# Kernel optimization log

Measured on AMD Instinct MI355X. Metric: run time of the kernel, lower is better.

## Reference

```python
import jax, jax.numpy as jnp
import numpy as np

N_SESS = 4096
N_TRIALS = 2048


def setup_inputs() -> dict:
    key = jax.random.key(0)
    k1, k2 = jax.random.split(key)
    # chose_left is a one-hot choice; chose_right = 1 - chose_left; outcome in {0,1}
    chose_left = jax.random.bernoulli(k1, 0.5, (N_SESS, N_TRIALS)).astype(jnp.float32)
    chose_right = 1.0 - chose_left
    outcome = jax.random.bernoulli(k2, 0.5, (N_SESS, N_TRIALS)).astype(jnp.float32)
    inp = jnp.stack([chose_left, chose_right, outcome], axis=-1)  # (n_sess, n_trials, 3)
    # raw logits; AlphaParam applies sigmoid. logit(0.8), logit(0.6)
    p_stay_raw = jnp.array([np.log(0.8 / 0.2)], dtype=jnp.float32)
    c_raw = jnp.array([np.log(0.6 / 0.4)], dtype=jnp.float32)
    return {"input": inp, "p_stay_raw": p_stay_raw, "c_raw": c_raw}


def _forward(inp, p_stay_raw, c_raw):
    p = jax.nn.sigmoid(p_stay_raw)[0]
    c = jax.nn.sigmoid(c_raw)[0]
    # With complement_c_rew=complement_c_diff=True, all four c params equal c.
    # ev_mat (4,2): rows = [left&rew, left&unrew, right&rew, right&unrew]
    col0 = 0.5 * jnp.stack([1 + c, 1 - c, 1 - c, 1 + c])
    col1 = 0.5 * jnp.stack([1 - c, 1 + c, 1 + c, 1 - c])
    ev_mat = jnp.stack([col0, col1], axis=1)  # (4, 2)
    trans_mat = 0.5 * jnp.stack([jnp.stack([1 + p, 1 - p]),
                                 jnp.stack([1 - p, 1 + p])])  # (2, 2)

    n_sess = inp.shape[0]
    init_state = jnp.full((n_sess, 2), 0.5, dtype=inp.dtype)

    def step(state, x):  # state: (n_sess, 2), x: (n_sess, 3)
        cl, cr, o = x[:, 0], x[:, 1], x[:, 2]
        sel = jnp.stack([cl * o, cl * (1 - o), cr * o, cr * (1 - o)], axis=1)  # (n_sess, 4)
        evidence = sel @ ev_mat            # (n_sess, 2)
        like = evidence * state            # (n_sess, 2)
        like_sum = like.sum(axis=1)        # (n_sess,)
        zero = like_sum == 0
        like = jnp.where(zero[:, None], state, like)
        like_sum = jnp.where(zero, 1.0, like_sum)
        norm_like = like / like_sum[:, None]
        new_state = norm_like @ trans_mat  # (n_sess, 2)
        return new_state, new_state

    # scan over trials (time axis); output stacked as (n_trials, n_sess, 2)
    _, out = jax.lax.scan(step, init_state, jnp.swapaxes(inp, 0, 1))
    return jnp.swapaxes(out, 0, 1)  # (n_sess, n_trials, 2)


def reference(input, p_stay_raw, c_raw):
    return _forward(input, p_stay_raw, c_raw)
```

## Files before the change

kernel.cpp:

```cpp
#include <hip/hip_runtime.h>
#include <cmath>


constexpr int NSESS = 4096;
constexpr int NTRIALS = 2048;
constexpr int LCH = 32;
constexpr int WAVES_PER_BLOCK = 4;

__global__ __launch_bounds__(256) void hmm_scan_kernel(
    const float* __restrict__ inp,
    const float* __restrict__ p_raw,
    const float* __restrict__ c_raw,
    float* __restrict__ out)
{
    const int lane = threadIdx.x & 63;
    const int wid  = threadIdx.x >> 6;
    const int sess = blockIdx.x * WAVES_PER_BLOCK + wid;
    if (sess >= NSESS) return;

    const float p = 1.0f / (1.0f + __expf(-p_raw[0]));
    const float c = 1.0f / (1.0f + __expf(-c_raw[0]));
    const float A = 0.5f * (1.0f + c), B = 0.5f * (1.0f - c);
    const float q = 0.5f * (1.0f + p), r = 0.5f * (1.0f - p);

    const float* x = inp + ((size_t)sess * NTRIALS + (size_t)lane * LCH) * 3;
    const float4* xv = reinterpret_cast<const float4*>(x);

    float e0c[LCH], e1c[LCH];
    float p00 = 1.f, p01 = 0.f, p10 = 0.f, p11 = 1.f;

    #pragma unroll
    for (int g = 0; g < LCH / 4; ++g) {
        float4 v0 = xv[3 * g + 0];
        float4 v1 = xv[3 * g + 1];
        float4 v2 = xv[3 * g + 2];
        float t[4][3] = {{v0.x, v0.y, v0.z}, {v0.w, v1.x, v1.y},
                         {v1.z, v1.w, v2.x}, {v2.y, v2.z, v2.w}};
        #pragma unroll
        for (int j = 0; j < 4; ++j) {
            float cl = t[j][0], cr = t[j][1], o = t[j][2];
            float s0 = cl * o, s1 = cl - s0, s2 = cr * o, s3 = cr - s2;
            float d0 = s0 + s3, d1 = s1 + s2;
            float e0 = d0 * A + d1 * B;
            float e1 = d0 * B + d1 * A;
            e0c[4 * g + j] = e0;
            e1c[4 * g + j] = e1;
            float m00, m01, m10, m11;
            if (e0 == 0.f && e1 == 0.f) { m00 = q; m01 = r; m10 = r; m11 = q; }
            else { m00 = e0 * q; m01 = e0 * r; m10 = e1 * r; m11 = e1 * q; }
            float n00 = p00 * m00 + p01 * m10;
            float n01 = p00 * m01 + p01 * m11;
            float n10 = p10 * m00 + p11 * m10;
            float n11 = p10 * m01 + p11 * m11;
            float inv = 1.f / (n00 + n01 + n10 + n11);
            p00 = n00 * inv; p01 = n01 * inv; p10 = n10 * inv; p11 = n11 * inv;
        }
    }

    #pragma unroll
    for (int d = 1; d < 64; d <<= 1) {
        float a00 = __shfl_up(p00, d);
        float a01 = __shfl_up(p01, d);
        float a10 = __shfl_up(p10, d);
        float a11 = __shfl_up(p11, d);
        if (lane >= d) {
            float n00 = a00 * p00 + a01 * p10;
            float n01 = a00 * p01 + a01 * p11;
            float n10 = a10 * p00 + a11 * p10;
            float n11 = a10 * p01 + a11 * p11;
            float inv = 1.f / (n00 + n01 + n10 + n11);
            p00 = n00 * inv; p01 = n01 * inv; p10 = n10 * inv; p11 = n11 * inv;
        }
    }

    float c00 = __shfl_up(p00, 1);
    float c01 = __shfl_up(p01, 1);
    float c10 = __shfl_up(p10, 1);
    float c11 = __shfl_up(p11, 1);
    float st0 = 0.5f, st1 = 0.5f;
    if (lane > 0) {
        float v0 = 0.5f * c00 + 0.5f * c10;
        float v1 = 0.5f * c01 + 0.5f * c11;
        float inv = 1.f / (v0 + v1);
        st0 = v0 * inv; st1 = v1 * inv;
    }

    float4* yv = reinterpret_cast<float4*>(
        out + ((size_t)sess * NTRIALS + (size_t)lane * LCH) * 2);

    #pragma unroll
    for (int i = 0; i < LCH; i += 2) {
        float a0, a1, b0, b1;
        {
            float l0 = st0 * e0c[i], l1 = st1 * e1c[i];
            float ls = l0 + l1;
            if (ls == 0.f) { l0 = st0; l1 = st1; ls = 1.f; }
            float inv = 1.f / ls;
            float n0 = l0 * inv, n1 = l1 * inv;
            st0 = n0 * q + n1 * r;
            st1 = n0 * r + n1 * q;
            a0 = st0; a1 = st1;
        }
        {
            float l0 = st0 * e0c[i + 1], l1 = st1 * e1c[i + 1];
            float ls = l0 + l1;
            if (ls == 0.f) { l0 = st0; l1 = st1; ls = 1.f; }
            float inv = 1.f / ls;
            float n0 = l0 * inv, n1 = l1 * inv;
            st0 = n0 * q + n1 * r;
            st1 = n0 * r + n1 * q;
            b0 = st0; b1 = st1;
        }
        yv[i >> 1] = make_float4(a0, a1, b0, b1);
    }
}

extern "C" void kernel_launch(void* const* d_in, const int* in_sizes, int n_in,
                              void* d_out, int out_size, void* d_ws, size_t ws_size,
                              hipStream_t stream) {
    const float* inp   = (const float*)d_in[0];
    const float* p_raw = (const float*)d_in[1];
    const float* c_raw = (const float*)d_in[2];
    float* out = (float*)d_out;

    dim3 grid(NSESS / WAVES_PER_BLOCK);
    dim3 block(64 * WAVES_PER_BLOCK);
    hmm_scan_kernel<<<grid, block, 0, stream>>>(inp, p_raw, c_raw, out);
}
```

Measured before the change: 197.8 us.

## Split each session across a block and stage input and output through LDS

Each block now handles one session, with four waves each scanning a quarter of the trials at eight trials per lane instead of 32. Chunk totals are combined across waves through shared memory. Input is loaded into LDS with coalesced float4 reads, and output is transposed through LDS so global stores are coalesced. The per-step renormalisation in the chunk product and forward pass is deferred to the output, which trims divides but relies on short chunks to avoid underflow.

```diff
diff --git a/kernel.cpp b/kernel.cpp
--- a/kernel.cpp
+++ b/kernel.cpp
@@ -2,49 +2,56 @@
 #include <cmath>
 
 
-constexpr int NSESS = 4096;
+constexpr int NSESS   = 4096;
 constexpr int NTRIALS = 2048;
-constexpr int LCH = 32;
-constexpr int WAVES_PER_BLOCK = 4;
+constexpr int WAVES   = 4;
+constexpr int THREADS = WAVES * 64;
+constexpr int TPW     = NTRIALS / WAVES;
+constexpr int LCH     = TPW / 64;
+constexpr int IN_F4   = NTRIALS * 3 / 4;
+constexpr int OUT_F4  = NTRIALS * 2 / 4;
 
-__global__ __launch_bounds__(256) void hmm_scan_kernel(
+__global__ __launch_bounds__(THREADS) void hmm_kernel(
     const float* __restrict__ inp,
     const float* __restrict__ p_raw,
     const float* __restrict__ c_raw,
     float* __restrict__ out)
 {
-    const int lane = threadIdx.x & 63;
-    const int wid  = threadIdx.x >> 6;
-    const int sess = blockIdx.x * WAVES_PER_BLOCK + wid;
-    if (sess >= NSESS) return;
+    __shared__ float4 lds[IN_F4];
+    __shared__ float  lds_tot[WAVES][4];
+
+    const int t    = threadIdx.x;
+    const int lane = t & 63;
+    const int w    = t >> 6;
+    const int sess = blockIdx.x;
 
     const float p = 1.0f / (1.0f + __expf(-p_raw[0]));
     const float c = 1.0f / (1.0f + __expf(-c_raw[0]));
     const float A = 0.5f * (1.0f + c), B = 0.5f * (1.0f - c);
     const float q = 0.5f * (1.0f + p), r = 0.5f * (1.0f - p);
 
-    const float* x = inp + ((size_t)sess * NTRIALS + (size_t)lane * LCH) * 3;
-    const float4* xv = reinterpret_cast<const float4*>(x);
+    const float4* g_in = reinterpret_cast<const float4*>(inp) + (size_t)sess * IN_F4;
+    #pragma unroll
+    for (int k = 0; k < IN_F4 / THREADS; ++k)
+        lds[k * THREADS + t] = g_in[k * THREADS + t];
+    __syncthreads();
 
     float e0c[LCH], e1c[LCH];
     float p00 = 1.f, p01 = 0.f, p10 = 0.f, p11 = 1.f;
-
-    #pragma unroll
-    for (int g = 0; g < LCH / 4; ++g) {
-        float4 v0 = xv[3 * g + 0];
-        float4 v1 = xv[3 * g + 1];
-        float4 v2 = xv[3 * g + 2];
-        float t[4][3] = {{v0.x, v0.y, v0.z}, {v0.w, v1.x, v1.y},
-                         {v1.z, v1.w, v2.x}, {v2.y, v2.z, v2.w}};
+    {
+        float4 v[LCH * 3 / 4];
+        const int base = w * (TPW * 3 / 4) + lane * (LCH * 3 / 4);
         #pragma unroll
-        for (int j = 0; j < 4; ++j) {
-            float cl = t[j][0], cr = t[j][1], o = t[j][2];
-            float s0 = cl * o, s1 = cl - s0, s2 = cr * o, s3 = cr - s2;
-            float d0 = s0 + s3, d1 = s1 + s2;
+        for (int k = 0; k < LCH * 3 / 4; ++k) v[k] = lds[base + k];
+        const float* f = reinterpret_cast<const float*>(v);
+        #pragma unroll
+        for (int i = 0; i < LCH; ++i) {
+            float cl = f[3 * i], cr = f[3 * i + 1], o = f[3 * i + 2];
+            float d0 = cl * o + cr * (1.f - o);
+            float d1 = cl * (1.f - o) + cr * o;
             float e0 = d0 * A + d1 * B;
             float e1 = d0 * B + d1 * A;
-            e0c[4 * g + j] = e0;
-            e1c[4 * g + j] = e1;
+            e0c[i] = e0; e1c[i] = e1;
             float m00, m01, m10, m11;
             if (e0 == 0.f && e1 == 0.f) { m00 = q; m01 = r; m10 = r; m11 = q; }
             else { m00 = e0 * q; m01 = e0 * r; m10 = e1 * r; m11 = e1 * q; }
@@ -52,8 +59,7 @@
             float n01 = p00 * m01 + p01 * m11;
             float n10 = p10 * m00 + p11 * m10;
             float n11 = p10 * m01 + p11 * m11;
-            float inv = 1.f / (n00 + n01 + n10 + n11);
-            p00 = n00 * inv; p01 = n01 * inv; p10 = n10 * inv; p11 = n11 * inv;
+            p00 = n00; p01 = n01; p10 = n10; p11 = n11;
         }
     }
 
@@ -73,45 +79,63 @@
         }
     }
 
+    if (lane == 63) {
+        lds_tot[w][0] = p00; lds_tot[w][1] = p01;
+        lds_tot[w][2] = p10; lds_tot[w][3] = p11;
+    }
+    __syncthreads();
+
+    float v0 = 0.5f, v1 = 0.5f;
+    for (int ww = 0; ww < w; ++ww) {
+        float t00 = lds_tot[ww][0], t01 = lds_tot[ww][1];
+        float t10 = lds_tot[ww][2], t11 = lds_tot[ww][3];
+        float n0 = v0 * t00 + v1 * t10;
+        float n1 = v0 * t01 + v1 * t11;
+        float inv = 1.f / (n0 + n1);
+        v0 = n0 * inv; v1 = n1 * inv;
+    }
     float c00 = __shfl_up(p00, 1);
     float c01 = __shfl_up(p01, 1);
     float c10 = __shfl_up(p10, 1);
     float c11 = __shfl_up(p11, 1);
-    float st0 = 0.5f, st1 = 0.5f;
+    float u0 = v0, u1 = v1;
     if (lane > 0) {
-        float v0 = 0.5f * c00 + 0.5f * c10;
-        float v1 = 0.5f * c01 + 0.5f * c11;
-        float inv = 1.f / (v0 + v1);
-        st0 = v0 * inv; st1 = v1 * inv;
+        float n0 = v0 * c00 + v1 * c10;
+        float n1 = v0 * c01 + v1 * c11;
+        float inv = 1.f / (n0 + n1);
+        u0 = n0 * inv; u1 = n1 * inv;
     }
 
-    float4* yv = reinterpret_cast<float4*>(
-        out + ((size_t)sess * NTRIALS + (size_t)lane * LCH) * 2);
-
+    float4* lds_out = lds;
     #pragma unroll
     for (int i = 0; i < LCH; i += 2) {
         float a0, a1, b0, b1;
         {
-            float l0 = st0 * e0c[i], l1 = st1 * e1c[i];
-            float ls = l0 + l1;
-            if (ls == 0.f) { l0 = st0; l1 = st1; ls = 1.f; }
-            float inv = 1.f / ls;
-            float n0 = l0 * inv, n1 = l1 * inv;
-            st0 = n0 * q + n1 * r;
-            st1 = n0 * r + n1 * q;
-            a0 = st0; a1 = st1;
+            float w0 = u0 * e0c[i], w1 = u1 * e1c[i];
+            if (w0 + w1 == 0.f) { w0 = u0; w1 = u1; }
+            float n0 = w0 * q + w1 * r;
+            float n1 = w0 * r + w1 * q;
+            float inv = 1.f / (n0 + n1);
+            a0 = n0 * inv; a1 = n1 * inv;
+            u0 = n0; u1 = n1;
         }
         {
-            float l0 = st0 * e0c[i + 1], l1 = st1 * e1c[i + 1];
-            float ls = l0 + l1;
-            if (ls == 0.f) { l0 = st0; l1 = st1; ls = 1.f; }
-            float inv = 1.f / ls;
-            float n0 = l0 * inv, n1 = l1 * inv;
-            st0 = n0 * q + n1 * r;
-            st1 = n0 * r + n1 * q;
-            b0 = st0; b1 = st1;
+            float w0 = u0 * e0c[i + 1], w1 = u1 * e1c[i + 1];
+            if (w0 + w1 == 0.f) { w0 = u0; w1 = u1; }
+            float n0 = w0 * q + w1 * r;
+            float n1 = w0 * r + w1 * q;
+            float inv = 1.f / (n0 + n1);
+            b0 = n0 * inv; b1 = n1 * inv;
+            u0 = n0; u1 = n1;
         }
-        yv[i >> 1] = make_float4(a0, a1, b0, b1);
+        lds_out[w * 256 + (i >> 1) * 64 + lane] = make_float4(a0, a1, b0, b1);
+    }
+    __syncthreads();
+
+    float4* g_out = reinterpret_cast<float4*>(out) + (size_t)sess * OUT_F4;
+    #pragma unroll
+    for (int k = 0; k < OUT_F4 / THREADS; ++k) {
+        g_out[k * 256 + t] = lds_out[k * 256 + (t & 3) * 64 + (t >> 2)];
     }
 }
 
@@ -123,7 +147,5 @@
     const float* c_raw = (const float*)d_in[2];
     float* out = (float*)d_out;
 
-    dim3 grid(NSESS / WAVES_PER_BLOCK);
-    dim3 block(64 * WAVES_PER_BLOCK);
-    hmm_scan_kernel<<<grid, block, 0, stream>>>(inp, p_raw, c_raw, out);
+    hmm_kernel<<<dim3(NSESS), dim3(THREADS), 0, stream>>>(inp, p_raw, c_raw, out);
 }
```

After: 166.9 us. 1.19x faster.
